# Kernel tuning notes

Measured on AMD Instinct MI355X. Metric: run time of the kernel, lower is better.

## Reference

```python
import jax, jax.numpy as jnp
import numpy as np

C_Z = 128
C_HIDDEN = 32
N_HEAD = 4
HC = N_HEAD * C_HIDDEN  # 128
LN_EPS = 1e-5


def setup_inputs() -> dict:
    key = jax.random.key(0)
    ks = jax.random.split(key, 8)
    b, n = 1, 256
    s = 1.0 / np.sqrt(C_Z)
    return {
        "z_ij": jax.random.normal(ks[0], (b, n, n, C_Z), dtype=jnp.float32),
        "ln_gamma": jnp.ones((C_Z,), dtype=jnp.float32),
        "ln_beta": jnp.zeros((C_Z,), dtype=jnp.float32),
        "Wq": jax.random.normal(ks[1], (C_Z, HC), dtype=jnp.float32) * s,
        "Wk": jax.random.normal(ks[2], (C_Z, HC), dtype=jnp.float32) * s,
        "Wv": jax.random.normal(ks[3], (C_Z, HC), dtype=jnp.float32) * s,
        "Wb": jax.random.normal(ks[4], (C_Z, N_HEAD), dtype=jnp.float32) * s,
        "Wg": jax.random.normal(ks[5], (C_Z, HC), dtype=jnp.float32) * s,
        "Wout": jax.random.normal(ks[6], (HC, C_Z), dtype=jnp.float32) * (1.0 / np.sqrt(HC)),
    }


def reference(z_ij, ln_gamma, ln_beta, Wq, Wk, Wv, Wb, Wg, Wout):
    b, n, _, _ = z_ij.shape
    # LayerNorm over c_z
    mu = jnp.mean(z_ij, axis=-1, keepdims=True)
    var = jnp.var(z_ij, axis=-1, keepdims=True)
    z = (z_ij - mu) * jax.lax.rsqrt(var + LN_EPS) * ln_gamma + ln_beta

    def heads(x):  # [b,i,j,hc] -> [b,i,j,h,d]
        return x.reshape(b, n, n, N_HEAD, C_HIDDEN)

    q = heads(z @ Wq)
    k = heads(z @ Wk)
    v = heads(z @ Wv)
    bias = z @ Wb                      # [b,i,j,h]
    g = jax.nn.sigmoid(heads(z @ Wg))  # [b,i,j,h,d]

    scores = jnp.einsum('bijhd,bikhd->bijkh', q, k) / np.sqrt(C_HIDDEN)
    scores = scores + bias[:, None]    # bias[b, j, k, h] broadcast over i
    a = jax.nn.softmax(scores, axis=-2)  # over k
    o = jnp.einsum('bijkh,bikhd->bijhd', a, v)
    o = (g * o).reshape(b, n, n, HC)
    return o @ Wout
```

## Files before the change

### kernel.cpp

```cpp
#include <hip/hip_runtime.h>

typedef _Float16 f16x8 __attribute__((ext_vector_type(8)));
typedef _Float16 f16x2 __attribute__((ext_vector_type(2)));
typedef float f32x4 __attribute__((ext_vector_type(4)));

#define MFMA16(a, b, c) __builtin_amdgcn_mfma_f32_16x16x32_f16(a, b, c, 0, 0, 0)

#define NROW 65536
#define SEGB 16777216ull
#define LOG2E 1.4426950408889634f

__global__ __launch_bounds__(256) void k_ln(
    const float* __restrict__ z, const float* __restrict__ gamma,
    const float* __restrict__ beta, const float* __restrict__ Wb,
    const float* __restrict__ Wq, const float* __restrict__ Wk,
    const float* __restrict__ Wv, const float* __restrict__ Wg,
    const float* __restrict__ Wout,
    _Float16* __restrict__ zln, float* __restrict__ biasT,
    _Float16* __restrict__ WtAll)
{
  __shared__ _Float16 sw[32 * 136];
  int bid = blockIdx.x;
  if (bid < 16384) {
    int lane = threadIdx.x & 63;
    int w = threadIdx.x >> 6;
    int row = bid * 4 + w;
    float2 v = ((const float2*)(z + (size_t)row * 128))[lane];
    float s = v.x + v.y;
    #pragma unroll
    for (int m = 1; m < 64; m <<= 1) s += __shfl_xor(s, m);
    float mu = s * 0.0078125f;
    float dx = v.x - mu, dy = v.y - mu;
    float q = dx * dx + dy * dy;
    #pragma unroll
    for (int m = 1; m < 64; m <<= 1) q += __shfl_xor(q, m);
    float rs = rsqrtf(q * 0.0078125f + 1e-5f);
    float2 g2 = ((const float2*)gamma)[lane];
    float2 b2 = ((const float2*)beta)[lane];
    float y0 = dx * rs * g2.x + b2.x;
    float y1 = dy * rs * g2.y + b2.y;
    f16x2 pr; pr.x = (_Float16)y0; pr.y = (_Float16)y1;
    *(f16x2*)(zln + (size_t)row * 128 + 2 * lane) = pr;
  } else if (bid < 16384 + 20) {
    int t = bid - 16384;
    int mat = t >> 2, n0 = (t & 3) * 32;
    const float* src = (mat == 0) ? Wq : (mat == 1) ? Wk : (mat == 2) ? Wv
                       : (mat == 3) ? Wg : Wout;
    _Float16* dst = WtAll + ((mat == 4) ? 5 : mat) * 16384;
    for (int it = 0; it < 16; ++it) {
      int e = threadIdx.x + it * 256;
      int c = e >> 5, j = e & 31;
      sw[j * 136 + c] = (_Float16)src[c * 128 + n0 + j];
    }
    __syncthreads();
    for (int it = 0; it < 2; ++it) {
      int ch = threadIdx.x + it * 256;
      int n = ch >> 4, k8 = (ch & 15) * 8;
      *(int4*)(dst + (n0 + n) * 128 + k8) = *(const int4*)&sw[n * 136 + k8];
    }
  } else {
    _Float16* dst = WtAll + 4 * 16384;
    for (int e = threadIdx.x; e < 16384; e += 256) {
      int n = e >> 7, k = e & 127;
      dst[e] = (n < 4) ? (_Float16)Wb[k * 4 + n] : (_Float16)0.f;
    }
  }
}

__global__ __launch_bounds__(256) void k_proj(
    const _Float16* __restrict__ A, const _Float16* __restrict__ WtAll,
    _Float16* __restrict__ Qb, _Float16* __restrict__ Kb,
    _Float16* __restrict__ Vb, _Float16* __restrict__ Gb,
    float* __restrict__ biasT)
{
  __shared__ _Float16 sA[128 * 136];
  __shared__ _Float16 sB[128 * 136];
  int e = blockIdx.x;
  int xcd = e & 7;
  int t = e >> 3;
  int by = t % 5;
  int g = t / 5;
  int m0 = (g * 8 + xcd) * 128;
  const _Float16* Bt = WtAll + by * 16384;
  _Float16* outp = (by == 0) ? Qb : (by == 1) ? Kb : (by == 2) ? Vb : Gb;
  int tid = threadIdx.x;
  for (int it = 0; it < 8; ++it) {
    int ch = tid + it * 256;
    int r = ch >> 4, c8 = (ch & 15) * 8;
    *(int4*)&sA[r * 136 + c8] = *(const int4*)(A + (size_t)(m0 + r) * 128 + c8);
    *(int4*)&sB[r * 136 + c8] = *(const int4*)(Bt + r * 128 + c8);
  }
  __syncthreads();
  int lane = tid & 63, w = tid >> 6;
  int mw = (w >> 1) * 64, nw = (w & 1) * 64;
  int lr = lane & 15, lg = lane >> 4;
  int ntm = (by == 4) ? 1 : 4;
  f32x4 z4 = {0.f, 0.f, 0.f, 0.f};
  f32x4 acc[4][4];
  #pragma unroll
  for (int mt = 0; mt < 4; ++mt)
    #pragma unroll
    for (int nt = 0; nt < 4; ++nt) acc[mt][nt] = z4;
  #pragma unroll
  for (int k0 = 0; k0 < 128; k0 += 32) {
    f16x8 af[4], bf[4];
    #pragma unroll
    for (int mt = 0; mt < 4; ++mt)
      af[mt] = *(const f16x8*)&sA[(mw + mt * 16 + lr) * 136 + k0 + lg * 8];
    #pragma unroll
    for (int nt = 0; nt < 4; ++nt)
      if (nt < ntm)
        bf[nt] = *(const f16x8*)&sB[(nw + nt * 16 + lr) * 136 + k0 + lg * 8];
    #pragma unroll
    for (int mt = 0; mt < 4; ++mt)
      #pragma unroll
      for (int nt = 0; nt < 4; ++nt)
        if (nt < ntm)
          acc[mt][nt] = MFMA16(af[mt], bf[nt], acc[mt][nt]);
  }
  if (by == 4) {
    if (nw == 0 && lr < 4) {
      #pragma unroll
      for (int mt = 0; mt < 4; ++mt)
        #pragma unroll
        for (int r = 0; r < 4; ++r) {
          int row = m0 + mw + mt * 16 + lg * 4 + r;
          int lowk = row & 255;
          int pos = (row & ~255) | ((lowk & 15) << 4) | (lowk >> 4);
          biasT[(size_t)lr * NROW + pos] = acc[mt][0][r] * LOG2E;
        }
    }
    return;
  }
  bool sig = (by == 3);
  #pragma unroll
  for (int mt = 0; mt < 4; ++mt)
    #pragma unroll
    for (int nt = 0; nt < 4; ++nt)
      #pragma unroll
      for (int r = 0; r < 4; ++r) {
        int row = m0 + mw + mt * 16 + lg * 4 + r;
        int col = nw + nt * 16 + lr;
        float v = acc[mt][nt][r];
        if (sig) v = 1.0f / (1.0f + __expf(-v));
        outp[(size_t)row * 128 + col] = (_Float16)v;
      }
}

__global__ __launch_bounds__(256) void k_attn(
    const _Float16* __restrict__ Qb, const _Float16* __restrict__ Kb,
    const _Float16* __restrict__ Vb, const _Float16* __restrict__ Gb,
    const float* __restrict__ biasT, _Float16* __restrict__ OG)
{
  __shared__ _Float16 sV[32 * 256];
  __shared__ _Float16 sP[64 * 256];
  int i = blockIdx.x, h = blockIdx.y;
  int tid = threadIdx.x;
  size_t base = ((size_t)i * 256) * 128 + h * 32;
  for (int it = 0; it < 4; ++it) {
    int ch = tid + it * 256;
    int k = ch >> 2, d8 = (ch & 3) * 8;
    f16x8 tv = *(const f16x8*)(Vb + base + (size_t)k * 128 + d8);
    int k2 = ((k & 15) << 4) | (k >> 4);
    int c2 = k2 >> 3, e2 = k2 & 7;
    #pragma unroll
    for (int jj = 0; jj < 8; ++jj) {
      int d = d8 + jj;
      int p = c2 ^ (d & 7);
      sV[d * 256 + p * 8 + e2] = tv[jj];
    }
  }
  __syncthreads();
  int lane = tid & 63, w = tid >> 6;
  int lr = lane & 15, lg = lane >> 4;
  const float scale = 0.2550348858f;
  f32x4 z4 = {0.f, 0.f, 0.f, 0.f};
  const _Float16* Kp = Kb + base;
  for (int pass = 0; pass < 4; ++pass) {
    int jbase = pass * 64;
    int jq = jbase + w * 16 + lr;
    f16x8 aq = *(const f16x8*)(Qb + base + (size_t)jq * 128 + lg * 8);
    f32x4 sacc[16];
    __builtin_amdgcn_s_setprio(1);
    #pragma unroll
    for (int kt = 0; kt < 16; ++kt) {
      int r = kt * 16 + lr;
      f16x8 bk = *(const f16x8*)(Kp + (size_t)r * 128 + lg * 8);
      sacc[kt] = MFMA16(aq, bk, z4);
    }
    __builtin_amdgcn_s_setprio(0);
    float rinv4[4];
    #pragma unroll
    for (int r = 0; r < 4; ++r) {
      int j = jbase + w * 16 + lg * 4 + r;
      const float* brow = biasT + (size_t)h * NROW + (size_t)j * 256 + lr * 16;
      float4 b4[4];
      #pragma unroll
      for (int m = 0; m < 4; ++m) b4[m] = ((const float4*)brow)[m];
      float mx = -1e30f;
      #pragma unroll
      for (int kt = 0; kt < 16; ++kt) {
        float bb = ((const float*)&b4[kt >> 2])[kt & 3];
        float sv = sacc[kt][r] * scale + bb;
        sacc[kt][r] = sv;
        mx = fmaxf(mx, sv);
      }
      #pragma unroll
      for (int msk = 1; msk < 16; msk <<= 1) mx = fmaxf(mx, __shfl_xor(mx, msk));
      float sum = 0.f;
      f16x8 h0, h1;
      #pragma unroll
      for (int kt = 0; kt < 16; ++kt) {
        float pv = exp2f(sacc[kt][r] - mx);
        sum += pv;
        if (kt < 8) h0[kt] = (_Float16)pv;
        else        h1[kt - 8] = (_Float16)pv;
      }
      #pragma unroll
      for (int msk = 1; msk < 16; msk <<= 1) sum += __shfl_xor(sum, msk);
      rinv4[r] = 1.0f / sum;
      int row = w * 16 + lg * 4 + r;
      *(f16x8*)&sP[row * 256 + ((2 * lr) ^ (row & 7)) * 8] = h0;
      *(f16x8*)&sP[row * 256 + ((2 * lr + 1) ^ (row & 7)) * 8] = h1;
    }
    f32x4 oacc[2] = {z4, z4};
    int prow = w * 16 + lr;
    #pragma unroll
    for (int ks = 0; ks < 8; ++ks) {
      int c = ks * 4 + lg;
      f16x8 ap = *(const f16x8*)&sP[prow * 256 + (c ^ (prow & 7)) * 8];
      __builtin_amdgcn_s_setprio(1);
      #pragma unroll
      for (int nt = 0; nt < 2; ++nt) {
        int d = nt * 16 + lr;
        f16x8 bv = *(const f16x8*)&sV[d * 256 + (c ^ (d & 7)) * 8];
        oacc[nt] = MFMA16(ap, bv, oacc[nt]);
      }
      __builtin_amdgcn_s_setprio(0);
    }
    #pragma unroll
    for (int nt = 0; nt < 2; ++nt)
      #pragma unroll
      for (int r = 0; r < 4; ++r) {
        int j = jbase + w * 16 + lg * 4 + r;
        int d = nt * 16 + lr;
        size_t idx = base + (size_t)j * 128 + d;
        float g = (float)Gb[idx];
        OG[idx] = (_Float16)(oacc[nt][r] * rinv4[r] * g);
      }
  }
}

__global__ __launch_bounds__(256) void k_outp(
    const _Float16* __restrict__ A, const _Float16* __restrict__ Bt,
    float* __restrict__ out)
{
  __shared__ _Float16 sA[128 * 136];
  __shared__ _Float16 sB[128 * 136];
  int m0 = blockIdx.x * 128;
  int tid = threadIdx.x;
  for (int it = 0; it < 8; ++it) {
    int ch = tid + it * 256;
    int r = ch >> 4, c8 = (ch & 15) * 8;
    *(int4*)&sA[r * 136 + c8] = *(const int4*)(A + (size_t)(m0 + r) * 128 + c8);
    *(int4*)&sB[r * 136 + c8] = *(const int4*)(Bt + r * 128 + c8);
  }
  __syncthreads();
  int lane = tid & 63, w = tid >> 6;
  int mw = (w >> 1) * 64, nw = (w & 1) * 64;
  int lr = lane & 15, lg = lane >> 4;
  f32x4 z4 = {0.f, 0.f, 0.f, 0.f};
  f32x4 acc[4][4];
  #pragma unroll
  for (int mt = 0; mt < 4; ++mt)
    #pragma unroll
    for (int nt = 0; nt < 4; ++nt) acc[mt][nt] = z4;
  #pragma unroll
  for (int k0 = 0; k0 < 128; k0 += 32) {
    f16x8 af[4], bf[4];
    #pragma unroll
    for (int mt = 0; mt < 4; ++mt)
      af[mt] = *(const f16x8*)&sA[(mw + mt * 16 + lr) * 136 + k0 + lg * 8];
    #pragma unroll
    for (int nt = 0; nt < 4; ++nt)
      bf[nt] = *(const f16x8*)&sB[(nw + nt * 16 + lr) * 136 + k0 + lg * 8];
    #pragma unroll
    for (int mt = 0; mt < 4; ++mt)
      #pragma unroll
      for (int nt = 0; nt < 4; ++nt)
        acc[mt][nt] = MFMA16(af[mt], bf[nt], acc[mt][nt]);
  }
  #pragma unroll
  for (int mt = 0; mt < 4; ++mt)
    #pragma unroll
    for (int nt = 0; nt < 4; ++nt)
      #pragma unroll
      for (int r = 0; r < 4; ++r) {
        int row = m0 + mw + mt * 16 + lg * 4 + r;
        int col = nw + nt * 16 + lr;
        out[(size_t)row * 128 + col] = acc[mt][nt][r];
      }
}

extern "C" void kernel_launch(void* const* d_in, const int* in_sizes, int n_in,
                              void* d_out, int out_size, void* d_ws, size_t ws_size,
                              hipStream_t stream) {
  (void)in_sizes; (void)n_in; (void)out_size; (void)ws_size;
  const float* z    = (const float*)d_in[0];
  const float* gam  = (const float*)d_in[1];
  const float* bet  = (const float*)d_in[2];
  const float* Wq   = (const float*)d_in[3];
  const float* Wk   = (const float*)d_in[4];
  const float* Wv   = (const float*)d_in[5];
  const float* Wb   = (const float*)d_in[6];
  const float* Wg   = (const float*)d_in[7];
  const float* Wout = (const float*)d_in[8];

  char* ws = (char*)d_ws;
  _Float16* zln   = (_Float16*)(ws);
  _Float16* Qb    = (_Float16*)(ws + SEGB);
  _Float16* Kb    = (_Float16*)(ws + SEGB * 2);
  _Float16* Vb    = (_Float16*)(ws + SEGB * 3);
  _Float16* Gb    = (_Float16*)(ws + SEGB * 4);
  float*    biasT = (float*)   (ws + SEGB * 5);
  _Float16* WtAll = (_Float16*)(ws + SEGB * 5 + 1048576);

  k_ln<<<16405, 256, 0, stream>>>(z, gam, bet, Wb, Wq, Wk, Wv, Wg, Wout,
                                  zln, biasT, WtAll);
  k_proj<<<2560, 256, 0, stream>>>(zln, WtAll, Qb, Kb, Vb, Gb, biasT);
  k_attn<<<dim3(256, 4), 256, 0, stream>>>(Qb, Kb, Vb, Gb, biasT, zln);
  k_outp<<<512, 256, 0, stream>>>(zln, WtAll + 5 * 16384, (float*)d_out);
}
```

Measured before the change: 197.6 us.

## Chunk softmax-PV in attention with per-wave small P tile and interleaved MFMA

Restructures the attention softmax/PV stage so that exponentials are computed in four chunks of 64 keys, each written to a small per-wave padded LDS tile and immediately consumed by PV MFMAs, instead of writing the full 64x256 P tile first. The V layout in shared memory is re-permuted to match the new key ordering, and the row sum reduction is deferred to the end. This shrinks LDS use, which may raise occupancy, and interleaves exp/VALU work with MFMA. The cost is a more intricate index mapping and possible LDS bank conflicts or hazards within the wave tile, since no barrier separates the writes from the reads.

```diff
diff --git a/kernel.cpp b/kernel.cpp
--- a/kernel.cpp
+++ b/kernel.cpp
@@ -1,6 +1,7 @@
 #include <hip/hip_runtime.h>
 
 typedef _Float16 f16x8 __attribute__((ext_vector_type(8)));
+typedef _Float16 f16x4 __attribute__((ext_vector_type(4)));
 typedef _Float16 f16x2 __attribute__((ext_vector_type(2)));
 typedef float f32x4 __attribute__((ext_vector_type(4)));
 
@@ -153,7 +154,7 @@
     const float* __restrict__ biasT, _Float16* __restrict__ OG)
 {
   __shared__ _Float16 sV[32 * 256];
-  __shared__ _Float16 sP[64 * 256];
+  __shared__ _Float16 sPw[4 * 16 * 68];
   int i = blockIdx.x, h = blockIdx.y;
   int tid = threadIdx.x;
   size_t base = ((size_t)i * 256) * 128 + h * 32;
@@ -161,13 +162,12 @@
     int ch = tid + it * 256;
     int k = ch >> 2, d8 = (ch & 3) * 8;
     f16x8 tv = *(const f16x8*)(Vb + base + (size_t)k * 128 + d8);
-    int k2 = ((k & 15) << 4) | (k >> 4);
-    int c2 = k2 >> 3, e2 = k2 & 7;
+    int p = ((k >> 6) << 6) | ((k & 15) << 2) | ((k >> 4) & 3);
+    int pc = p >> 3, pe = p & 7;
     #pragma unroll
     for (int jj = 0; jj < 8; ++jj) {
       int d = d8 + jj;
-      int p = c2 ^ (d & 7);
-      sV[d * 256 + p * 8 + e2] = tv[jj];
+      sV[d * 256 + ((pc ^ (d & 7)) * 8) + pe] = tv[jj];
     }
   }
   __syncthreads();
@@ -176,6 +176,7 @@
   const float scale = 0.2550348858f;
   f32x4 z4 = {0.f, 0.f, 0.f, 0.f};
   const _Float16* Kp = Kb + base;
+  _Float16* spw = sPw + w * (16 * 68);
   for (int pass = 0; pass < 4; ++pass) {
     int jbase = pass * 64;
     int jq = jbase + w * 16 + lr;
@@ -189,7 +190,7 @@
       sacc[kt] = MFMA16(aq, bk, z4);
     }
     __builtin_amdgcn_s_setprio(0);
-    float rinv4[4];
+    float mx4[4];
     #pragma unroll
     for (int r = 0; r < 4; ++r) {
       int j = jbase + w * 16 + lg * 4 + r;
@@ -207,36 +208,47 @@
       }
       #pragma unroll
       for (int msk = 1; msk < 16; msk <<= 1) mx = fmaxf(mx, __shfl_xor(mx, msk));
-      float sum = 0.f;
-      f16x8 h0, h1;
-      #pragma unroll
-      for (int kt = 0; kt < 16; ++kt) {
-        float pv = exp2f(sacc[kt][r] - mx);
-        sum += pv;
-        if (kt < 8) h0[kt] = (_Float16)pv;
-        else        h1[kt - 8] = (_Float16)pv;
-      }
-      #pragma unroll
-      for (int msk = 1; msk < 16; msk <<= 1) sum += __shfl_xor(sum, msk);
-      rinv4[r] = 1.0f / sum;
-      int row = w * 16 + lg * 4 + r;
-      *(f16x8*)&sP[row * 256 + ((2 * lr) ^ (row & 7)) * 8] = h0;
-      *(f16x8*)&sP[row * 256 + ((2 * lr + 1) ^ (row & 7)) * 8] = h1;
-    }
+      mx4[r] = mx;
+    }
+    float sum4[4] = {0.f, 0.f, 0.f, 0.f};
     f32x4 oacc[2] = {z4, z4};
-    int prow = w * 16 + lr;
-    #pragma unroll
-    for (int ks = 0; ks < 8; ++ks) {
-      int c = ks * 4 + lg;
-      f16x8 ap = *(const f16x8*)&sP[prow * 256 + (c ^ (prow & 7)) * 8];
-      __builtin_amdgcn_s_setprio(1);
-      #pragma unroll
-      for (int nt = 0; nt < 2; ++nt) {
-        int d = nt * 16 + lr;
-        f16x8 bv = *(const f16x8*)&sV[d * 256 + (c ^ (d & 7)) * 8];
-        oacc[nt] = MFMA16(ap, bv, oacc[nt]);
-      }
-      __builtin_amdgcn_s_setprio(0);
+    #pragma unroll
+    for (int q = 0; q < 4; ++q) {
+      #pragma unroll
+      for (int r = 0; r < 4; ++r) {
+        float p0 = exp2f(sacc[4 * q + 0][r] - mx4[r]);
+        float p1 = exp2f(sacc[4 * q + 1][r] - mx4[r]);
+        float p2 = exp2f(sacc[4 * q + 2][r] - mx4[r]);
+        float p3 = exp2f(sacc[4 * q + 3][r] - mx4[r]);
+        sum4[r] += (p0 + p1) + (p2 + p3);
+        f16x4 pk;
+        pk.x = (_Float16)p0; pk.y = (_Float16)p1;
+        pk.z = (_Float16)p2; pk.w = (_Float16)p3;
+        int row = lg * 4 + r;
+        *(f16x4*)&spw[row * 68 + lr * 4] = pk;
+      }
+      #pragma unroll
+      for (int kk = 0; kk < 2; ++kk) {
+        int cq = kk * 4 + lg;
+        f16x8 ap = *(const f16x8*)&spw[lr * 68 + cq * 8];
+        int c = q * 8 + cq;
+        __builtin_amdgcn_s_setprio(1);
+        #pragma unroll
+        for (int nt = 0; nt < 2; ++nt) {
+          int d = nt * 16 + lr;
+          f16x8 bv = *(const f16x8*)&sV[d * 256 + ((c ^ (d & 7)) * 8)];
+          oacc[nt] = MFMA16(ap, bv, oacc[nt]);
+        }
+        __builtin_amdgcn_s_setprio(0);
+      }
+    }
+    float rinv4[4];
+    #pragma unroll
+    for (int r = 0; r < 4; ++r) {
+      float s = sum4[r];
+      #pragma unroll
+      for (int msk = 1; msk < 16; msk <<= 1) s += __shfl_xor(s, msk);
+      rinv4[r] = 1.0f / s;
     }
     #pragma unroll
     for (int nt = 0; nt < 2; ++nt)
```

Result: slower. 211.3 us (+6.9%).
